# Kernel optimization log

Measured on AMD Instinct MI355X. Metric: run time of the kernel, lower is better.

Reference implementation:

```python
import jax, jax.numpy as jnp
import numpy as np

EPS = 1e-6

def _sigma(x):
    # ELU+1 feature map used by Infini-Attention / linear attention
    return jax.nn.elu(x) + 1.0

def setup_inputs() -> dict:
    key = jax.random.key(0)
    ks = jax.random.split(key, 8)
    B, S, H, D = 2, 4096, 2048, 128
    sc = 1.0 / np.sqrt(H)
    return {
        "hidden_states": jax.random.normal(ks[0], (B, S, H), jnp.float32),
        "w_q": jax.random.normal(ks[1], (D, H), jnp.float32) * sc,
        "w_k": jax.random.normal(ks[2], (D, H), jnp.float32) * sc,
        "w_v": jax.random.normal(ks[3], (D, H), jnp.float32) * sc,
        "w_o": jax.random.normal(ks[4], (H, D), jnp.float32) * (1.0 / np.sqrt(D)),
        "gate": jnp.zeros((1,), jnp.float32),
        "M": jax.random.normal(ks[5], (D, D), jnp.float32),
        "z": jax.random.uniform(ks[6], (D,), jnp.float32) + 0.5,
    }

def reference(hidden_states, w_q, w_k, w_v, w_o, gate, M, z):
    # projections (torch Linear: x @ W^T)
    q = jnp.einsum('bsh,dh->bsd', hidden_states, w_q)
    k = jnp.einsum('bsh,dh->bsd', hidden_states, w_k)
    v = jnp.einsum('bsh,dh->bsd', hidden_states, w_v)

    # --- compressive memory retrieve: sigma(q) M / (sigma(q) . z) ---
    sq = _sigma(q)                                   # [B,S,D]
    mem_num = jnp.einsum('bsd,de->bse', sq, M)       # [B,S,D]
    mem_den = jnp.einsum('bsd,d->bs', sq, z) + EPS
    memory_output = mem_num / mem_den[..., None]

    # --- causal linear attention (cumulative-sum, non-softmax) ---
    pq, pk = _sigma(q), _sigma(k)
    kv_cum = jnp.cumsum(jnp.einsum('bsd,bse->bsde', pk, v), axis=1)  # [B,S,D,D] running state
    k_cum = jnp.cumsum(pk, axis=1)                                    # [B,S,D]
    num = jnp.einsum('bsd,bsde->bse', pq, kv_cum)
    den = jnp.einsum('bsd,bsd->bs', pq, k_cum) + EPS
    local_output = num / den[..., None]

    g = jax.nn.sigmoid(gate)                         # [1], broadcasts
    output = g * memory_output + (1.0 - g) * local_output

    # --- delta-rule memory update ---
    sk = _sigma(k)
    v_ret = jnp.einsum('bsd,de->bse', sk, M) / (jnp.einsum('bsd,d->bs', sk, z) + EPS)[..., None]
    M_new = M + jnp.einsum('bsd,bse->de', sk, v - v_ret)
    z_new = z + jnp.sum(sk, axis=(0, 1))

    out = jnp.einsum('bsd,hd->bsh', output, w_o)
    return out, M_new, z_new
```

## Files before the change

### kernel.cpp

```cpp
#include <hip/hip_runtime.h>
#include <hip/hip_bf16.h>
#include <math.h>

#define DI __device__ __forceinline__

typedef __bf16 bf16x8 __attribute__((ext_vector_type(8)));
typedef float  f32x4  __attribute__((ext_vector_type(4)));

static constexpr int   Bsz  = 2, Ssz = 4096, Hsz = 2048, Dsz = 128;
static constexpr int   Nrow = Bsz * Ssz;
static constexpr int   NCH  = Nrow / 128;
static constexpr int   CPB  = Ssz / 128;
static constexpr int   WN   = Dsz * Hsz;
static constexpr float EPSF = 1e-6f;

static constexpr size_t WQKV_OFF = 0;
static constexpr size_t WO_OFF   = (size_t)3*WN*2;
static constexpr size_t MB_OFF   = WO_OFF + (size_t)WN*2;
static constexpr size_t MBT_OFF  = MB_OFF + 32768;
static constexpr size_t QB_OFF   = MBT_OFF + 32768;
static constexpr size_t KB_OFF   = QB_OFF + (size_t)Nrow*Dsz*2;
static constexpr size_t VB_OFF   = KB_OFF + (size_t)Nrow*Dsz*2;
static constexpr size_t PB_OFF   = VB_OFF + (size_t)Nrow*Dsz*2;
static constexpr size_t ACC_OFF  = PB_OFF + (size_t)Nrow*Dsz*2;
static constexpr size_t KV_OFF   = ACC_OFF;
static constexpr size_t KVP_OFF  = ACC_OFF + (size_t)4*1024*1024;
static constexpr size_t MPART_OFF= ACC_OFF + (size_t)6*1024*1024;
static constexpr size_t KSUM_OFF = ACC_OFF + (size_t)10*1024*1024;
static constexpr size_t KPRE_OFF = KSUM_OFF + 32768;

DI float b2f(unsigned short u) {
    union { float f; unsigned int i; } x; x.i = ((unsigned int)u) << 16; return x.f;
}
DI unsigned short f2b(float f) {
    __bf16 h = (__bf16)f; return __builtin_bit_cast(unsigned short, h);
}
DI float sig_elu(float x) { return x > 0.f ? x + 1.f : expf(x); }

DI f32x4 MFMA(bf16x8 a, bf16x8 b, f32x4 c) {
    return __builtin_amdgcn_mfma_f32_16x16x32_bf16(a, b, c, 0, 0, 0);
}
template<int NB>
DI void zaccg(f32x4 (&acc)[4][NB]) {
    f32x4 zz = {0.f, 0.f, 0.f, 0.f};
    #pragma unroll
    for (int i = 0; i < 4; i++)
        #pragma unroll
        for (int j = 0; j < NB; j++) acc[i][j] = zz;
}
template<int NB>
DI void zacc2(f32x4 (&acc)[2][NB]) {
    f32x4 zz = {0.f, 0.f, 0.f, 0.f};
    #pragma unroll
    for (int i = 0; i < 2; i++)
        #pragma unroll
        for (int j = 0; j < NB; j++) acc[i][j] = zz;
}

DI void gll16(const void* g, void* l) {
    __builtin_amdgcn_global_load_lds((const __attribute__((address_space(1))) void*)g,
                                     (__attribute__((address_space(3))) void*)l, 16, 0, 0);
}

DI int swzR(int r, int kc, int R) { return (kc*R + (r ^ (kc & 7))) * 8; }

template<int NKS, int NB>
DI void mmg(const unsigned short* A, const unsigned short* Bm, f32x4 (&acc)[4][NB],
            int wm, int wn, int quad, int lr) {
    #pragma unroll
    for (int ks = 0; ks < NKS; ks++) {
        bf16x8 a[4], b[NB];
        #pragma unroll
        for (int mb = 0; mb < 4; mb++)
            a[mb] = *(const bf16x8*)&A[swzR(wm*64 + mb*16 + lr, ks*4 + quad, 128)];
        #pragma unroll
        for (int nb = 0; nb < NB; nb++)
            b[nb] = *(const bf16x8*)&Bm[swzR(wn*(NB*16) + nb*16 + lr, ks*4 + quad, NB*32)];
        #pragma unroll
        for (int mb = 0; mb < 4; mb++)
            #pragma unroll
            for (int nb = 0; nb < NB; nb++)
                acc[mb][nb] = MFMA(a[mb], b[nb], acc[mb][nb]);
    }
}

template<int NKS, int NB>
DI void mmg64(const unsigned short* A, const unsigned short* Bm, f32x4 (&acc)[2][NB],
              int wm, int wn, int quad, int lr) {
    #pragma unroll
    for (int ks = 0; ks < NKS; ks++) {
        bf16x8 a[2], b[NB];
        #pragma unroll
        for (int mb = 0; mb < 2; mb++)
            a[mb] = *(const bf16x8*)&A[swzR(wm*32 + mb*16 + lr, ks*4 + quad, 64)];
        #pragma unroll
        for (int nb = 0; nb < NB; nb++)
            b[nb] = *(const bf16x8*)&Bm[swzR(wn*(NB*16) + nb*16 + lr, ks*4 + quad, NB*32)];
        #pragma unroll
        for (int mb = 0; mb < 2; mb++)
            #pragma unroll
            for (int nb = 0; nb < NB; nb++)
                acc[mb][nb] = MFMA(a[mb], b[nb], acc[mb][nb]);
    }
}

template<int R>
DI void stage_dir(unsigned short* dst, const unsigned short* src, int src_ld, int tid) {
    #pragma unroll
    for (int i = 0; i < R/16; i++) {
        int s = tid + i*256; int r = s >> 4, kc = s & 15;
        *(uint4*)&dst[swzR(r, kc, R)] = *(const uint4*)(src + (size_t)r*src_ld + kc*8);
    }
}

DI void stage_T128(unsigned short* dst, const unsigned short* src, int src_ld, int tid) {
    #pragma unroll
    for (int i = 0; i < 8; i++) {
        int s = tid + i*256;
        int rw = (s & 15) + ((s >> 8) << 4);
        int c0 = ((s >> 4) & 15) * 8;
        unsigned short tmp[8];
        *(uint4*)tmp = *(const uint4*)(src + (size_t)rw*src_ld + c0);
        #pragma unroll
        for (int j = 0; j < 8; j++)
            dst[swzR(c0 + j, rw >> 3, 128) + (rw & 7)] = tmp[j];
    }
}

DI void stage_T64(unsigned short* dst, const unsigned short* src, int src_ld, int colOff, int tid) {
    #pragma unroll
    for (int i = 0; i < 4; i++) {
        int s = tid + i*256;
        int rw = s >> 3;
        int c0 = (s & 7) * 8;
        unsigned short tmp[8];
        *(uint4*)tmp = *(const uint4*)(src + (size_t)rw*src_ld + colOff + c0);
        #pragma unroll
        for (int j = 0; j < 8; j++)
            dst[swzR(c0 + j, rw >> 3, 64) + (rw & 7)] = tmp[j];
    }
}

DI void stage_T32(unsigned short* dst, const unsigned short* src, int src_ld, int colOff, int tid) {
    #pragma unroll
    for (int i = 0; i < 2; i++) {
        int s = tid + i*256;
        int rw = (s & 15) + ((s >> 6) << 4);
        int c0 = ((s >> 4) & 3) * 8;
        unsigned short tmp[8];
        *(uint4*)tmp = *(const uint4*)(src + (size_t)rw*src_ld + colOff + c0);
        #pragma unroll
        for (int j = 0; j < 8; j++)
            dst[swzR(c0 + j, rw >> 3, 32) + (rw & 7)] = tmp[j];
    }
}


__global__ void k_cvt_w(const float* __restrict__ wq, const float* __restrict__ wk,
                        const float* __restrict__ wv, const float* __restrict__ wo,
                        const float* __restrict__ M, unsigned short* __restrict__ dst,
                        unsigned short* __restrict__ MbT)
{
    int gid = blockIdx.x*256 + threadIdx.x;
    if (gid >= (4*WN + 16384)/4) return;
    int e = gid*4;
    const float* src; int rel;
    if      (e < WN)     { src = wq; rel = e; }
    else if (e < 2*WN)   { src = wk; rel = e - WN; }
    else if (e < 3*WN)   { src = wv; rel = e - 2*WN; }
    else if (e < 4*WN)   { src = wo; rel = e - 3*WN; }
    else                 { src = M;  rel = e - 4*WN; }
    float4 v = *(const float4*)(src + rel);
    const float* vf = (const float*)&v;
    unsigned short o[4];
    #pragma unroll
    for (int j = 0; j < 4; j++) o[j] = f2b(vf[j]);
    *(uint2*)&dst[e] = *(const uint2*)o;
    if (e >= 4*WN) {
        #pragma unroll
        for (int j = 0; j < 4; j++) {
            int d = (rel + j) >> 7, ee = (rel + j) & 127;
            MbT[ee*128 + d] = o[j];
        }
    }
}

__global__ __launch_bounds__(256, 2) void k_gemm_qkv(
    const float* __restrict__ X, const unsigned short* __restrict__ W,
    unsigned short* __restrict__ AccB)
{
    __shared__ unsigned short lA[64*64];
    __shared__ unsigned short lB[384*64];
    const int tid = threadIdx.x;
    const int row0 = blockIdx.x * 64;
    const int kb   = blockIdx.y * 512;
    const int wave = tid >> 6, lane = tid & 63;
    const int quad = lane >> 4, lr = lane & 15;

    const int cA0 = tid, cA1 = tid + 256;
    const int rA0 = cA0 >> 3, kA0 = cA0 & 7;
    const int rA1 = cA1 >> 3, kA1 = cA1 & 7;
    const float* pA0 = X + (size_t)(row0 + rA0)*Hsz + kA0*8;
    const float* pA1 = X + (size_t)(row0 + rA1)*Hsz + kA1*8;
    unsigned short* wA0 = &lA[(rA0*8 + (kA0 ^ (rA0 & 7)))*8];
    unsigned short* wA1 = &lA[(rA1*8 + (kA1 ^ (rA1 & 7)))*8];

    f32x4 acc[4][6]; zaccg(acc);

    float4 a00 = *(const float4*)(pA0 + kb);
    float4 a01 = *(const float4*)(pA0 + kb + 4);
    float4 a10 = *(const float4*)(pA1 + kb);
    float4 a11 = *(const float4*)(pA1 + kb + 4);

    for (int kt = kb; kt < kb + 512; kt += 64) {
        #pragma unroll
        for (int i = 0; i < 12; i++) {
            int p = tid + i*256; int r = p >> 3; int kc = (p & 7) ^ (r & 7);
            gll16(W + (size_t)r*Hsz + kt + kc*8, &lB[p*8]);
        }
        {
            unsigned short o[8];
            const float* f0 = (const float*)&a00; const float* f1 = (const float*)&a01;
            #pragma unroll
            for (int j = 0; j < 4; j++) { o[j] = f2b(f0[j]); o[4+j] = f2b(f1[j]); }
            *(uint4*)wA0 = *(const uint4*)o;
            const float* f2 = (const float*)&a10; const float* f3 = (const float*)&a11;
            #pragma unroll
            for (int j = 0; j < 4; j++) { o[j] = f2b(f2[j]); o[4+j] = f2b(f3[j]); }
            *(uint4*)wA1 = *(const uint4*)o;
        }
        __syncthreads();
        if (kt + 64 < kb + 512) {
            a00 = *(const float4*)(pA0 + kt + 64);
            a01 = *(const float4*)(pA0 + kt + 64 + 4);
            a10 = *(const float4*)(pA1 + kt + 64);
            a11 = *(const float4*)(pA1 + kt + 64 + 4);
        }
        #pragma unroll
        for (int ks = 0; ks < 2; ks++) {
            bf16x8 a[4], b[6];
            #pragma unroll
            for (int mb = 0; mb < 4; mb++) {
                int r = mb*16 + lr;
                int c = (ks*4 + quad) ^ (r & 7);
                a[mb] = *(const bf16x8*)&lA[(r*8 + c)*8];
            }
            #pragma unroll
            for (int nb = 0; nb < 6; nb++) {
                int r = wave*96 + nb*16 + lr;
                int c = (ks*4 + quad) ^ (r & 7);
                b[nb] = *(const bf16x8*)&lB[(r*8 + c)*8];
            }
            #pragma unroll
            for (int mb = 0; mb < 4; mb++)
                #pragma unroll
                for (int nb = 0; nb < 6; nb++)
                    acc[mb][nb] = MFMA(a[mb], b[nb], acc[mb][nb]);
        }
        __syncthreads();
    }

    unsigned short* base = AccB + (size_t)blockIdx.y * 3 * Nrow * 128;
    #pragma unroll
    for (int mb = 0; mb < 4; mb++)
        #pragma unroll
        for (int nb = 0; nb < 6; nb++)
            #pragma unroll
            for (int rg = 0; rg < 4; rg++) {
                int s_ = mb*16 + quad*4 + rg;
                int n  = wave*96 + nb*16 + lr;
                int ct = n >> 7, e_ = n & 127;
                base[(size_t)ct*Nrow*128 + (size_t)(row0 + s_)*128 + e_] =
                    f2b(acc[mb][nb][rg]);
            }
}

__global__ void k_qkv_epi(const unsigned short* __restrict__ AccB,
                          unsigned short* __restrict__ Qb,
                          unsigned short* __restrict__ Kb, unsigned short* __restrict__ Vb)
{
    int gid = blockIdx.x*256 + threadIdx.x;
    int ct = gid / (Nrow*16);
    int off = (gid - ct*Nrow*16) * 8;
    float vs[8];
    #pragma unroll
    for (int j = 0; j < 8; j++) vs[j] = 0.f;
    #pragma unroll
    for (int s = 0; s < 4; s++) {
        uint4 u = *(const uint4*)&AccB[((size_t)s*3 + ct)*Nrow*128 + off];
        const unsigned short* us = (const unsigned short*)&u;
        #pragma unroll
        for (int j = 0; j < 8; j++) vs[j] += b2f(us[j]);
    }
    unsigned short o[8];
    if (ct < 2) {
        #pragma unroll
        for (int j = 0; j < 8; j++) o[j] = f2b(sig_elu(vs[j]));
    } else {
        #pragma unroll
        for (int j = 0; j < 8; j++) o[j] = f2b(vs[j]);
    }
    unsigned short* dst = (ct == 0) ? Qb : (ct == 1 ? Kb : Vb);
    *(uint4*)&dst[off] = *(const uint4*)o;
}

__global__ __launch_bounds__(256, 2) void k_delta_kv(
    const unsigned short* __restrict__ Kb, const unsigned short* __restrict__ Vb,
    const unsigned short* __restrict__ MbT, const float* __restrict__ z,
    float* __restrict__ KV, float* __restrict__ ksum, float* __restrict__ Mpart)
{
    __shared__ unsigned short b0[128*128];
    __shared__ unsigned short bA[64*128];
    __shared__ unsigned short b1a[32*128];
    __shared__ unsigned short b1b[32*128];
    __shared__ unsigned short b1c[32*128];
    __shared__ float den[128];
    const int tid = threadIdx.x;
    const int c = blockIdx.x, t0 = c*128;
    const int e0 = blockIdx.y * 32;
    const int dh = blockIdx.z;
    const int wave = tid >> 6, lane = tid & 63;
    const int wm = wave >> 1, wn = wave & 1, quad = lane >> 4, lr = lane & 15;

    stage_dir<128>(b0, Kb + (size_t)t0*Dsz, Dsz, tid);
    stage_T64(bA, Kb + (size_t)t0*Dsz, Dsz, dh*64, tid);
    stage_dir<32>(b1a, MbT + (size_t)e0*128, 128, tid);
    stage_T32(b1c, Vb + (size_t)t0*Dsz, Dsz, e0, tid);
    __syncthreads();

    f32x4 acc1[4][1]; zaccg(acc1);
    mmg<4,1>(b0, b1a, acc1, wm, wn, quad, lr);

    if (tid < 128) {
        float p = 0.f;
        for (int d = 0; d < 128; d++)
            p += b2f(b0[swzR(tid, d >> 3, 128) + (d & 7)]) * z[d];
        den[tid] = p + EPSF;
        if (e0 == 0 && dh == 0) {
            float q = 0.f;
            for (int t = 0; t < 128; t++)
                q += b2f(b0[swzR(t, tid >> 3, 128) + (tid & 7)]);
            ksum[(size_t)c*128 + tid] = q;
        }
    }
    __syncthreads();

    #pragma unroll
    for (int mb = 0; mb < 4; mb++)
        #pragma unroll
        for (int rg = 0; rg < 4; rg++) {
            int s_ = wm*64 + mb*16 + quad*4 + rg;
            int el = wn*16 + lr;
            float v = b2f(Vb[(size_t)(t0 + s_)*Dsz + e0 + el]);
            float w = v - acc1[mb][0][rg] / den[s_];
            b1b[swzR(el, s_ >> 3, 32) + (s_ & 7)] = f2b(w);
        }
    __syncthreads();

    f32x4 acc2[2][1]; zacc2(acc2);
    mmg64<4,1>(bA, b1b, acc2, wm, wn, quad, lr);
    f32x4 acc3[2][1]; zacc2(acc3);
    mmg64<4,1>(bA, b1c, acc3, wm, wn, quad, lr);
    #pragma unroll
    for (int mb = 0; mb < 2; mb++)
        #pragma unroll
        for (int rg = 0; rg < 4; rg++) {
            int d_ = dh*64 + wm*32 + mb*16 + quad*4 + rg;
            int el = wn*16 + lr;
            Mpart[(size_t)c*16384 + (size_t)d_*128 + e0 + el] = acc2[mb][0][rg];
            KV[(size_t)c*16384 + (size_t)d_*128 + e0 + el]    = acc3[mb][0][rg];
        }
}

__global__ void k_scan_final(
    const float* __restrict__ KV, const float* __restrict__ ksum,
    const float* __restrict__ M, const float* __restrict__ z,
    const float* __restrict__ Mpart, unsigned short* __restrict__ KVp,
    float* __restrict__ kpre, float* __restrict__ omz)
{
    int idx = blockIdx.x*256 + threadIdx.x;
    if (idx < 32768) {
        int batch = idx >> 14, ed = idx & 16383;
        float a = 0.f;
        #pragma unroll 8
        for (int i = 0; i < CPB; i++) {
            size_t cc = (size_t)(batch*CPB + i);
            KVp[cc*16384 + ed] = f2b(a);
            a += KV[cc*16384 + ed];
        }
    } else if (idx < 33024) {
        int j = idx - 32768; int batch = j >> 7, d = j & 127;
        float a = 0.f;
        #pragma unroll 8
        for (int i = 0; i < CPB; i++) {
            int cc = batch*CPB + i;
            kpre[cc*128 + d] = a;
            a += ksum[cc*128 + d];
        }
    } else if (idx < 49408) {
        int m = idx - 33024;
        float a = M[m];
        #pragma unroll 8
        for (int cc = 0; cc < NCH; cc++) a += Mpart[(size_t)cc*16384 + m];
        omz[m] = a;
    } else if (idx < 49536) {
        int d = idx - 49408;
        float a = z[d];
        #pragma unroll 8
        for (int cc = 0; cc < NCH; cc++) a += ksum[cc*128 + d];
        omz[16384 + d] = a;
    }
}

template<int H>
DI void attn_impl(const unsigned short* Qb, const unsigned short* KVp,
                  const float* kpre, const unsigned short* MbT,
                  const float* z, const float* gate,
                  const unsigned short* Kb, const unsigned short* Vb,
                  unsigned short* P,
                  unsigned short* b0q, unsigned short* b1,
                  unsigned short* bq0, unsigned short* bq1,
                  float* dmem, float* dl, float* rs,
                  int c, int e0, int tid)
{
    const int t0 = c*128;
    const int wave = tid >> 6, lane = tid & 63;
    const int wm = wave >> 1, wn = wave & 1, quad = lane >> 4, lr = lane & 15;
    constexpr int NBT = H ? 4 : 2;
    constexpr int NKV = H ? 4 : 2;

    if (tid < 64) rs[tid] = 0.f;
    stage_dir<64>(b0q, Qb + (size_t)(t0 + H*64)*Dsz, Dsz, tid);
    stage_dir<128>(b1, Kb + (size_t)t0*Dsz, Dsz, tid);
    stage_dir<32>(bq0, MbT + (size_t)e0*128, 128, tid);
    stage_T32(bq1, KVp + (size_t)c*16384, 128, e0, tid);
    __syncthreads();

    if (tid < 64) {
        float p = 0.f;
        for (int d = 0; d < 128; d++)
            p += b2f(b0q[swzR(tid, d >> 3, 64) + (d & 7)]) * z[d];
        dmem[tid] = p + EPSF;
    } else if (tid < 128) {
        int s_ = tid - 64; float p = 0.f;
        for (int d = 0; d < 128; d++)
            p += b2f(b0q[swzR(s_, d >> 3, 64) + (d & 7)]) * kpre[c*128 + d];
        dl[s_] = p;
    }
    f32x4 accM[2][1]; zacc2(accM);
    mmg64<4,1>(b0q, bq0, accM, wm, wn, quad, lr);
    f32x4 accN[2][1]; zacc2(accN);
    mmg64<4,1>(b0q, bq1, accN, wm, wn, quad, lr);
    f32x4 accS[2][NBT]; zacc2(accS);
    #pragma unroll
    for (int ks = 0; ks < 4; ks++) {
        bf16x8 a[2], b[NBT];
        #pragma unroll
        for (int mb = 0; mb < 2; mb++)
            a[mb] = *(const bf16x8*)&b0q[swzR(wm*32 + mb*16 + lr, ks*4 + quad, 64)];
        #pragma unroll
        for (int nb = 0; nb < NBT; nb++)
            b[nb] = *(const bf16x8*)&b1[swzR(wn*(NBT*16) + nb*16 + lr, ks*4 + quad, 128)];
        #pragma unroll
        for (int mb = 0; mb < 2; mb++)
            #pragma unroll
            for (int nb = 0; nb < NBT; nb++)
                accS[mb][nb] = MFMA(a[mb], b[nb], accS[mb][nb]);
    }
    __syncthreads();

    float g = 1.f / (1.f + expf(-gate[0]));
    f32x4 base[2][1];
    #pragma unroll
    for (int mb = 0; mb < 2; mb++)
        #pragma unroll
        for (int rg = 0; rg < 4; rg++) {
            int s_ = wm*32 + mb*16 + quad*4 + rg;
            base[mb][0][rg] = g * accM[mb][0][rg] / dmem[s_];
        }
    #pragma unroll
    for (int mb = 0; mb < 2; mb++)
        #pragma unroll
        for (int rg = 0; rg < 4; rg++) {
            int s_ = wm*32 + mb*16 + quad*4 + rg;
            int sa = H*64 + s_;
            float part = 0.f;
            #pragma unroll
            for (int nb = 0; nb < NBT; nb++) {
                int t_ = wn*(NBT*16) + nb*16 + lr;
                float v = (t_ <= sa) ? accS[mb][nb][rg] : 0.f;
                part += v;
                b1[swzR(s_, t_ >> 3, 64) + (t_ & 7)] = f2b(v);
            }
            #pragma unroll
            for (int m = 1; m < 16; m <<= 1) part += __shfl_xor(part, m, 64);
            if (lr == 0) atomicAdd(&rs[s_], part);
        }
    stage_T32(bq0, Vb + (size_t)t0*Dsz, Dsz, e0, tid);
    __syncthreads();

    f32x4 accV[2][1]; zacc2(accV);
    mmg64<NKV,1>(b1, bq0, accV, wm, wn, quad, lr);

    #pragma unroll
    for (int mb = 0; mb < 2; mb++)
        #pragma unroll
        for (int rg = 0; rg < 4; rg++) {
            int s_ = wm*32 + mb*16 + quad*4 + rg;
            int el = wn*16 + lr;
            float num = accN[mb][0][rg] + accV[mb][0][rg];
            float dd  = dl[s_] + rs[s_] + EPSF;
            float val = base[mb][0][rg] + (1.f - g) * num / dd;
            P[(size_t)(t0 + H*64 + s_)*Dsz + e0 + el] = f2b(val);
        }
}

__global__ __launch_bounds__(256, 2) void k_attn(
    const unsigned short* __restrict__ Qb, const unsigned short* __restrict__ KVp,
    const float* __restrict__ kpre, const unsigned short* __restrict__ MbT,
    const float* __restrict__ z, const float* __restrict__ gate,
    const unsigned short* __restrict__ Kb, const unsigned short* __restrict__ Vb,
    unsigned short* __restrict__ P)
{
    __shared__ unsigned short b0q[64*128];
    __shared__ unsigned short b1[128*128];
    __shared__ unsigned short bq0[32*128];
    __shared__ unsigned short bq1[32*128];
    __shared__ float dmem[64], dl[64], rs[64];
    const int c = blockIdx.x, e0 = blockIdx.y * 32, tid = threadIdx.x;
    if (blockIdx.z == 0)
        attn_impl<0>(Qb, KVp, kpre, MbT, z, gate, Kb, Vb, P,
                     b0q, b1, bq0, bq1, dmem, dl, rs, c, e0, tid);
    else
        attn_impl<1>(Qb, KVp, kpre, MbT, z, gate, Kb, Vb, P,
                     b0q, b1, bq0, bq1, dmem, dl, rs, c, e0, tid);
}

__global__ __launch_bounds__(256, 2) void k_gemm_out(
    const unsigned short* __restrict__ P, const unsigned short* __restrict__ Wo,
    float* __restrict__ out)
{
    __shared__ unsigned short b0[128*128];
    __shared__ unsigned short b1[128*128];
    const int tid = threadIdx.x;
    const int row0 = blockIdx.x*128, n0 = blockIdx.y*128;
    const int wave = tid >> 6, lane = tid & 63;
    const int wm = wave >> 1, wn = wave & 1, quad = lane >> 4, lr = lane & 15;

    #pragma unroll
    for (int i = 0; i < 8; i++) {
        int p = tid + i*256; int r = p >> 4; int kc = (p & 15) ^ (r & 15);
        gll16(P + (size_t)(row0 + r)*Dsz + kc*8, &b0[p*8]);
    }
    #pragma unroll
    for (int i = 0; i < 8; i++) {
        int p = tid + i*256; int r = p >> 4; int kc = (p & 15) ^ (r & 15);
        gll16(Wo + (size_t)(n0 + r)*Dsz + kc*8, &b1[p*8]);
    }
    __syncthreads();

    f32x4 acc[4][4]; zaccg(acc);
    #pragma unroll
    for (int ks = 0; ks < 4; ks++) {
        bf16x8 a[4], b[4];
        #pragma unroll
        for (int mb = 0; mb < 4; mb++) {
            int r = wm*64 + mb*16 + lr;
            a[mb] = *(const bf16x8*)&b0[(r*16 + ((ks*4 + quad) ^ (r & 15)))*8];
        }
        #pragma unroll
        for (int nb = 0; nb < 4; nb++) {
            int r = wn*64 + nb*16 + lr;
            b[nb] = *(const bf16x8*)&b1[(r*16 + ((ks*4 + quad) ^ (r & 15)))*8];
        }
        #pragma unroll
        for (int mb = 0; mb < 4; mb++)
            #pragma unroll
            for (int nb = 0; nb < 4; nb++)
                acc[mb][nb] = MFMA(a[mb], b[nb], acc[mb][nb]);
    }
    #pragma unroll
    for (int mb = 0; mb < 4; mb++)
        #pragma unroll
        for (int nb = 0; nb < 4; nb++)
            #pragma unroll
            for (int rg = 0; rg < 4; rg++) {
                int s_ = wm*64 + mb*16 + quad*4 + rg;
                int e_ = wn*64 + nb*16 + lr;
                out[(size_t)(row0 + s_)*Hsz + n0 + e_] = acc[mb][nb][rg];
            }
}

extern "C" void kernel_launch(void* const* d_in, const int* in_sizes, int n_in,
                              void* d_out, int out_size, void* d_ws, size_t ws_size,
                              hipStream_t stream)
{
    const float* X    = (const float*)d_in[0];
    const float* wq   = (const float*)d_in[1];
    const float* wk   = (const float*)d_in[2];
    const float* wv   = (const float*)d_in[3];
    const float* wo   = (const float*)d_in[4];
    const float* gate = (const float*)d_in[5];
    const float* M    = (const float*)d_in[6];
    const float* z    = (const float*)d_in[7];

    char* ws = (char*)d_ws;
    unsigned short* Wfull = (unsigned short*)(ws + WQKV_OFF);
    unsigned short* Wo_b  = (unsigned short*)(ws + WO_OFF);
    unsigned short* MbT   = (unsigned short*)(ws + MBT_OFF);
    unsigned short* Qb    = (unsigned short*)(ws + QB_OFF);
    unsigned short* Kb    = (unsigned short*)(ws + KB_OFF);
    unsigned short* Vb    = (unsigned short*)(ws + VB_OFF);
    unsigned short* Pb    = (unsigned short*)(ws + PB_OFF);
    unsigned short* AccB  = (unsigned short*)(ws + ACC_OFF);
    float* KV    = (float*)(ws + KV_OFF);
    unsigned short* KVp = (unsigned short*)(ws + KVP_OFF);
    float* Mpart = (float*)(ws + MPART_OFF);
    float* ksum  = (float*)(ws + KSUM_OFF);
    float* kpre  = (float*)(ws + KPRE_OFF);

    float* outp   = (float*)d_out;
    float* out_mz = outp + (size_t)Nrow*Hsz;

    k_cvt_w<<<((4*WN + 16384)/4 + 255)/256, 256, 0, stream>>>(wq, wk, wv, wo, M, Wfull, MbT);
    k_gemm_qkv<<<dim3(Nrow/64, 4), 256, 0, stream>>>(X, Wfull, AccB);
    k_qkv_epi<<<(3*Nrow*16)/256, 256, 0, stream>>>(AccB, Qb, Kb, Vb);
    k_delta_kv<<<dim3(NCH, 4, 2), 256, 0, stream>>>(Kb, Vb, MbT, z, KV, ksum, Mpart);
    k_scan_final<<<194, 256, 0, stream>>>(KV, ksum, M, z, Mpart, KVp, kpre, out_mz);
    k_attn<<<dim3(NCH, 4, 2), 256, 0, stream>>>(Qb, KVp, kpre, MbT, z, gate, Kb, Vb, Pb);
    k_gemm_out<<<dim3(Nrow/128, Hsz/128), 256, 0, stream>>>(Pb, Wo_b, outp);
}
```

Baseline: 178.4 us.

## Drop split-K in QKV GEMM and fuse sigma epilogue into it

The QKV projection GEMM no longer splits K four ways into bf16 partial buffers that a separate epilogue kernel sums. Each block now covers 32 rows over the full hidden dimension and writes Q, K, V directly, applying the ELU+1 feature map in registers. This removes the partial-sum buffer round trip through memory and one kernel launch, and accumulates fully in fp32 instead of summing bf16-rounded partials. In exchange the grid shrinks to 256 blocks with smaller M tiles, so each block rereads the whole weight slab, and there is less parallelism and less reuse per LDS load.

After: 189.3 us. 6.1% more time.

```diff
diff --git a/kernel.cpp b/kernel.cpp
--- a/kernel.cpp
+++ b/kernel.cpp
@@ -22,11 +22,11 @@
 static constexpr size_t KB_OFF   = QB_OFF + (size_t)Nrow*Dsz*2;
 static constexpr size_t VB_OFF   = KB_OFF + (size_t)Nrow*Dsz*2;
 static constexpr size_t PB_OFF   = VB_OFF + (size_t)Nrow*Dsz*2;
-static constexpr size_t ACC_OFF  = PB_OFF + (size_t)Nrow*Dsz*2;
-static constexpr size_t KV_OFF   = ACC_OFF;
-static constexpr size_t KVP_OFF  = ACC_OFF + (size_t)4*1024*1024;
-static constexpr size_t MPART_OFF= ACC_OFF + (size_t)6*1024*1024;
-static constexpr size_t KSUM_OFF = ACC_OFF + (size_t)10*1024*1024;
+static constexpr size_t SCR_OFF  = PB_OFF + (size_t)Nrow*Dsz*2;
+static constexpr size_t KV_OFF   = SCR_OFF;
+static constexpr size_t KVP_OFF  = SCR_OFF + (size_t)4*1024*1024;
+static constexpr size_t MPART_OFF= SCR_OFF + (size_t)6*1024*1024;
+static constexpr size_t KSUM_OFF = SCR_OFF + (size_t)10*1024*1024;
 static constexpr size_t KPRE_OFF = KSUM_OFF + 32768;
 
 DI float b2f(unsigned short u) {
@@ -110,20 +110,6 @@
     for (int i = 0; i < R/16; i++) {
         int s = tid + i*256; int r = s >> 4, kc = s & 15;
         *(uint4*)&dst[swzR(r, kc, R)] = *(const uint4*)(src + (size_t)r*src_ld + kc*8);
-    }
-}
-
-DI void stage_T128(unsigned short* dst, const unsigned short* src, int src_ld, int tid) {
-    #pragma unroll
-    for (int i = 0; i < 8; i++) {
-        int s = tid + i*256;
-        int rw = (s & 15) + ((s >> 8) << 4);
-        int c0 = ((s >> 4) & 15) * 8;
-        unsigned short tmp[8];
-        *(uint4*)tmp = *(const uint4*)(src + (size_t)rw*src_ld + c0);
-        #pragma unroll
-        for (int j = 0; j < 8; j++)
-            dst[swzR(c0 + j, rw >> 3, 128) + (rw & 7)] = tmp[j];
     }
 }
 
@@ -187,32 +173,26 @@
 
 __global__ __launch_bounds__(256, 2) void k_gemm_qkv(
     const float* __restrict__ X, const unsigned short* __restrict__ W,
-    unsigned short* __restrict__ AccB)
-{
-    __shared__ unsigned short lA[64*64];
+    unsigned short* __restrict__ Qb, unsigned short* __restrict__ Kb,
+    unsigned short* __restrict__ Vb)
+{
+    __shared__ unsigned short lA[32*64];
     __shared__ unsigned short lB[384*64];
     const int tid = threadIdx.x;
-    const int row0 = blockIdx.x * 64;
-    const int kb   = blockIdx.y * 512;
+    const int row0 = blockIdx.x * 32;
     const int wave = tid >> 6, lane = tid & 63;
     const int quad = lane >> 4, lr = lane & 15;
 
-    const int cA0 = tid, cA1 = tid + 256;
-    const int rA0 = cA0 >> 3, kA0 = cA0 & 7;
-    const int rA1 = cA1 >> 3, kA1 = cA1 & 7;
-    const float* pA0 = X + (size_t)(row0 + rA0)*Hsz + kA0*8;
-    const float* pA1 = X + (size_t)(row0 + rA1)*Hsz + kA1*8;
-    unsigned short* wA0 = &lA[(rA0*8 + (kA0 ^ (rA0 & 7)))*8];
-    unsigned short* wA1 = &lA[(rA1*8 + (kA1 ^ (rA1 & 7)))*8];
-
-    f32x4 acc[4][6]; zaccg(acc);
-
-    float4 a00 = *(const float4*)(pA0 + kb);
-    float4 a01 = *(const float4*)(pA0 + kb + 4);
-    float4 a10 = *(const float4*)(pA1 + kb);
-    float4 a11 = *(const float4*)(pA1 + kb + 4);
-
-    for (int kt = kb; kt < kb + 512; kt += 64) {
+    const int rA = tid >> 3, kA = tid & 7;
+    const float* pA = X + (size_t)(row0 + rA)*Hsz + kA*8;
+    unsigned short* wA = &lA[(rA*8 + (kA ^ (rA & 7)))*8];
+
+    f32x4 acc[2][6]; zacc2(acc);
+
+    float4 a0 = *(const float4*)(pA);
+    float4 a1 = *(const float4*)(pA + 4);
+
+    for (int kt = 0; kt < Hsz; kt += 64) {
         #pragma unroll
         for (int i = 0; i < 12; i++) {
             int p = tid + i*256; int r = p >> 3; int kc = (p & 7) ^ (r & 7);
@@ -220,27 +200,21 @@
         }
         {
             unsigned short o[8];
-            const float* f0 = (const float*)&a00; const float* f1 = (const float*)&a01;
+            const float* f0 = (const float*)&a0; const float* f1 = (const float*)&a1;
             #pragma unroll
             for (int j = 0; j < 4; j++) { o[j] = f2b(f0[j]); o[4+j] = f2b(f1[j]); }
-            *(uint4*)wA0 = *(const uint4*)o;
-            const float* f2 = (const float*)&a10; const float* f3 = (const float*)&a11;
-            #pragma unroll
-            for (int j = 0; j < 4; j++) { o[j] = f2b(f2[j]); o[4+j] = f2b(f3[j]); }
-            *(uint4*)wA1 = *(const uint4*)o;
+            *(uint4*)wA = *(const uint4*)o;
         }
         __syncthreads();
-        if (kt + 64 < kb + 512) {
-            a00 = *(const float4*)(pA0 + kt + 64);
-            a01 = *(const float4*)(pA0 + kt + 64 + 4);
-            a10 = *(const float4*)(pA1 + kt + 64);
-            a11 = *(const float4*)(pA1 + kt + 64 + 4);
+        if (kt + 64 < Hsz) {
+            a0 = *(const float4*)(pA + kt + 64);
+            a1 = *(const float4*)(pA + kt + 64 + 4);
         }
         #pragma unroll
         for (int ks = 0; ks < 2; ks++) {
-            bf16x8 a[4], b[6];
-            #pragma unroll
-            for (int mb = 0; mb < 4; mb++) {
+            bf16x8 a[2], b[6];
+            #pragma unroll
+            for (int mb = 0; mb < 2; mb++) {
                 int r = mb*16 + lr;
                 int c = (ks*4 + quad) ^ (r & 7);
                 a[mb] = *(const bf16x8*)&lA[(r*8 + c)*8];
@@ -252,7 +226,7 @@
                 b[nb] = *(const bf16x8*)&lB[(r*8 + c)*8];
             }
             #pragma unroll
-            for (int mb = 0; mb < 4; mb++)
+            for (int mb = 0; mb < 2; mb++)
                 #pragma unroll
                 for (int nb = 0; nb < 6; nb++)
                     acc[mb][nb] = MFMA(a[mb], b[nb], acc[mb][nb]);
@@ -260,48 +234,21 @@
         __syncthreads();
     }
 
-    unsigned short* base = AccB + (size_t)blockIdx.y * 3 * Nrow * 128;
-    #pragma unroll
-    for (int mb = 0; mb < 4; mb++)
-        #pragma unroll
-        for (int nb = 0; nb < 6; nb++)
+    #pragma unroll
+    for (int mb = 0; mb < 2; mb++)
+        #pragma unroll
+        for (int nb = 0; nb < 6; nb++) {
+            int n  = wave*96 + nb*16 + lr;
+            int ct = n >> 7, e_ = n & 127;
+            unsigned short* dst = (ct == 0) ? Qb : (ct == 1 ? Kb : Vb);
             #pragma unroll
             for (int rg = 0; rg < 4; rg++) {
                 int s_ = mb*16 + quad*4 + rg;
-                int n  = wave*96 + nb*16 + lr;
-                int ct = n >> 7, e_ = n & 127;
-                base[(size_t)ct*Nrow*128 + (size_t)(row0 + s_)*128 + e_] =
-                    f2b(acc[mb][nb][rg]);
+                float v = acc[mb][nb][rg];
+                if (ct < 2) v = sig_elu(v);
+                dst[(size_t)(row0 + s_)*128 + e_] = f2b(v);
             }
-}
-
-__global__ void k_qkv_epi(const unsigned short* __restrict__ AccB,
-                          unsigned short* __restrict__ Qb,
-                          unsigned short* __restrict__ Kb, unsigned short* __restrict__ Vb)
-{
-    int gid = blockIdx.x*256 + threadIdx.x;
-    int ct = gid / (Nrow*16);
-    int off = (gid - ct*Nrow*16) * 8;
-    float vs[8];
-    #pragma unroll
-    for (int j = 0; j < 8; j++) vs[j] = 0.f;
-    #pragma unroll
-    for (int s = 0; s < 4; s++) {
-        uint4 u = *(const uint4*)&AccB[((size_t)s*3 + ct)*Nrow*128 + off];
-        const unsigned short* us = (const unsigned short*)&u;
-        #pragma unroll
-        for (int j = 0; j < 8; j++) vs[j] += b2f(us[j]);
-    }
-    unsigned short o[8];
-    if (ct < 2) {
-        #pragma unroll
-        for (int j = 0; j < 8; j++) o[j] = f2b(sig_elu(vs[j]));
-    } else {
-        #pragma unroll
-        for (int j = 0; j < 8; j++) o[j] = f2b(vs[j]);
-    }
-    unsigned short* dst = (ct == 0) ? Qb : (ct == 1 ? Kb : Vb);
-    *(uint4*)&dst[off] = *(const uint4*)o;
+        }
 }
 
 __global__ __launch_bounds__(256, 2) void k_delta_kv(
@@ -612,7 +559,6 @@
     unsigned short* Kb    = (unsigned short*)(ws + KB_OFF);
     unsigned short* Vb    = (unsigned short*)(ws + VB_OFF);
     unsigned short* Pb    = (unsigned short*)(ws + PB_OFF);
-    unsigned short* AccB  = (unsigned short*)(ws + ACC_OFF);
     float* KV    = (float*)(ws + KV_OFF);
     unsigned short* KVp = (unsigned short*)(ws + KVP_OFF);
     float* Mpart = (float*)(ws + MPART_OFF);
@@ -623,8 +569,7 @@
     float* out_mz = outp + (size_t)Nrow*Hsz;
 
     k_cvt_w<<<((4*WN + 16384)/4 + 255)/256, 256, 0, stream>>>(wq, wk, wv, wo, M, Wfull, MbT);
-    k_gemm_qkv<<<dim3(Nrow/64, 4), 256, 0, stream>>>(X, Wfull, AccB);
-    k_qkv_epi<<<(3*Nrow*16)/256, 256, 0, stream>>>(AccB, Qb, Kb, Vb);
+    k_gemm_qkv<<<Nrow/32, 256, 0, stream>>>(X, Wfull, Qb, Kb, Vb);
     k_delta_kv<<<dim3(NCH, 4, 2), 256, 0, stream>>>(Kb, Vb, MbT, z, KV, ksum, Mpart);
     k_scan_final<<<194, 256, 0, stream>>>(KV, ksum, M, z, Mpart, KVp, kpre, out_mz);
     k_attn<<<dim3(NCH, 4, 2), 256, 0, stream>>>(Qb, KVp, kpre, MbT, z, gate, Kb, Vb, Pb);
```
